# Performance work log

Hardware: AMD Instinct MI355X
Metric: run time of the kernel (lower is better)

Reference implementation:

```python
import jax, jax.numpy as jnp
from jax import lax
import numpy as np

NC = 80      # classes
NM = 32      # mask coefficients
N = 8400     # anchors/boxes
H = 640; W = 640          # output canvas (img_shape)
MH = 160; MW = 160        # prototype mask resolution (img/4)
K = 100                   # max detections after NMS (fixed for jit)
CONF = 0.4
IOU_T = 0.7


def setup_inputs() -> dict:
    key = jax.random.key(0)
    k1, k2, k3, k4, k5, k6 = jax.random.split(key, 6)
    # well-formed boxes x1,y1,x2,y2 in pixel coords
    x1 = jax.random.uniform(k1, (1, 1, N), minval=0.0, maxval=float(W - 120))
    y1 = jax.random.uniform(k2, (1, 1, N), minval=0.0, maxval=float(H - 120))
    wh = jax.random.uniform(k3, (1, 2, N), minval=16.0, maxval=112.0)
    boxes = jnp.concatenate([x1, y1, x1 + wh[:, 0:1], y1 + wh[:, 1:2]], axis=1)
    cls = jax.random.uniform(k4, (1, NC, N), minval=0.0, maxval=0.6)  # some exceed CONF
    coeffs = jax.random.normal(k5, (1, NM, N)) * 0.5
    detect = jnp.concatenate([boxes, cls, coeffs], axis=1)   # [1, 4+NC+NM, N]
    segment = jax.random.normal(k6, (1, NM, MH, MW))
    return {"detect": detect, "segment": segment}


def _per_image(d, proto):
    mi = 4 + NC
    d = d.T                              # [N, 4+NC+NM]
    boxes = d[:, :4]                     # x1,y1,x2,y2
    cls = d[:, 4:mi]
    scores = jnp.max(cls, axis=1)
    cids = jnp.argmax(cls, axis=1)
    coeffs = d[:, mi:]                   # [N, NM]
    valid = scores >= CONF
    # sort by confidence descending (invalid last)
    order = jnp.argsort(jnp.where(valid, -scores, jnp.inf))
    b = boxes[order]; s = scores[order]; v = valid[order]
    c = cids[order]; co = coeffs[order]
    idx = jnp.arange(N)
    area = (b[:, 2] - b[:, 0]) * (b[:, 3] - b[:, 1])
    # greedy class-agnostic NMS (sequential over sorted boxes, vectorized inner)
    def nms_step(keep, i):
        bi = b[i]
        ix1 = jnp.maximum(bi[0], b[:, 0]); iy1 = jnp.maximum(bi[1], b[:, 1])
        ix2 = jnp.minimum(bi[2], b[:, 2]); iy2 = jnp.minimum(bi[3], b[:, 3])
        inter = jnp.maximum(ix2 - ix1, 0.0) * jnp.maximum(iy2 - iy1, 0.0)
        iou = inter / (area[i] + area - inter)
        sup = (iou >= IOU_T) & (idx > i) & keep[i]
        return keep & ~sup, None
    keep, _ = lax.scan(nms_step, v, idx)
    # mask-coefficient matmul for ALL boxes (as in source: masks @ segment_reshaped)
    mlog = co @ proto.reshape(NM, -1)    # [N, MH*MW]
    kept_scores = jnp.where(keep, s, -1.0)
    topv, topi = lax.top_k(kept_scores, K)   # first K survivors (already score-sorted)
    valid_k = topv >= CONF
    bk = b[topi]; ck = c[topi]
    prob = jax.nn.sigmoid(mlog[topi].reshape(K, MH, MW))
    hard = (prob > 0.5).astype(prob.dtype)               # binarize at mask res
    up = jax.image.resize(hard, (K, H, W), method="bilinear")  # upsample to canvas
    maskk = up > 0.0
    ysg = jnp.arange(H)[:, None]; xsg = jnp.arange(W)[None, :]
    onehot = jax.nn.one_hot(ck, NC, dtype=jnp.float32)   # [K, NC]
    bi = bk.astype(jnp.int32)
    # paint objects in descending-score order; each box region is overwritten
    def paint(canvas, inp):
        box, m, oh, vv = inp
        inbox = (xsg >= box[0]) & (xsg < box[2]) & (ysg >= box[1]) & (ysg < box[3]) & vv
        canvas = jnp.where(inbox[..., None],
                           jnp.where((m & inbox)[..., None], oh, 0.0),
                           canvas)
        return canvas, None
    canvas0 = jnp.zeros((H, W, NC), dtype=jnp.float32)
    canvas, _ = lax.scan(paint, canvas0, (bi, maskk, onehot, valid_k))
    return canvas


def reference(detect, segment):
    return jax.vmap(_per_image)(detect, segment)   # [B, H, W, NC]
```

## Files before the change

kernel.cpp:

```cpp
#include <hip/hip_runtime.h>

#define NCLS 80
#define NMK  32
#define NB   8400
#define MH_  160
#define MP   25600
#define IH   640
#define IW   640
#define KTOP 100
#define CONFT 0.4f
#define IOUT 0.7f
#define T_PRE 384
#define TW   (T_PRE/64)

__global__ __launch_bounds__(256) void k_prep(const float* __restrict__ det,
    float* __restrict__ key, int* __restrict__ cid, int* __restrict__ rank,
    int* __restrict__ nvp)
{
  int n = blockIdx.x*256 + threadIdx.x;
  bool valid = false;
  if (n < NB){
    float best = det[4*NB + n];
    int bc = 0;
    #pragma unroll 8
    for (int c = 1; c < NCLS; ++c){
      float v = det[(4+c)*NB + n];
      if (v > best){ best = v; bc = c; }
    }
    cid[n] = bc;
    valid = best >= CONFT;
    key[n] = valid ? -best : __builtin_inff();
    rank[n] = 0;
  }
  unsigned long long bal = __ballot(valid);
  if ((threadIdx.x & 63) == 0)
    nvp[blockIdx.x*4 + (threadIdx.x >> 6)] = (int)__popcll(bal);
}

__global__ __launch_bounds__(256) void k_rank(const float* __restrict__ key, int* __restrict__ rank)
{
  __shared__ float tk[256];
  int n = blockIdx.x*256 + threadIdx.x;
  float kn = (n < NB) ? key[n] : 0.f;
  int j0 = blockIdx.y * 263;
  int j1 = min(j0 + 263, NB);
  int part = 0;
  for (int t0 = j0; t0 < j1; t0 += 256){
    int j = t0 + threadIdx.x;
    tk[threadIdx.x] = (j < NB) ? key[j] : 0.f;
    __syncthreads();
    int lim = min(256, j1 - t0);
    for (int jj = 0; jj < lim; ++jj){
      float kj = tk[jj];
      int jg = t0 + jj;
      part += ((kj < kn) || (kj == kn && jg < n)) ? 1 : 0;
    }
    __syncthreads();
  }
  if (n < NB && part) atomicAdd(&rank[n], part);
}

__global__ __launch_bounds__(256) void k_scatter(const float* __restrict__ det,
    const int* __restrict__ cid, const int* __restrict__ rank,
    int* __restrict__ perm, int* __restrict__ scid, float4* __restrict__ sbox)
{
  int n = blockIdx.x*256 + threadIdx.x;
  if (n >= NB) return;
  int r = rank[n];
  perm[r] = n;
  scid[r] = cid[n];
  float4 b;
  b.x = det[0*NB + n]; b.y = det[1*NB + n];
  b.z = det[2*NB + n]; b.w = det[3*NB + n];
  sbox[r] = b;
}

__global__ __launch_bounds__(64) void k_supmat(const float4* __restrict__ sbox,
    unsigned long long* __restrict__ supmat)
{
  const int lane = threadIdx.x;
  const int ti = blockIdx.x;
  const int tj = blockIdx.y;
  float4 bj = sbox[tj*64 + lane];
  float aj = (bj.z - bj.x) * (bj.w - bj.y);
  float4 bi_all = sbox[ti*64 + lane];
  float ai_all  = (bi_all.z - bi_all.x) * (bi_all.w - bi_all.y);
  const int jg = tj*64 + lane;
  unsigned long long myrow = 0ull;
  #pragma unroll 4
  for (int ii = 0; ii < 64; ++ii){
    float bix = __shfl(bi_all.x, ii, 64);
    float biy = __shfl(bi_all.y, ii, 64);
    float biz = __shfl(bi_all.z, ii, 64);
    float biw = __shfl(bi_all.w, ii, 64);
    float ai  = __shfl(ai_all,  ii, 64);
    float ix1 = fmaxf(bix, bj.x), iy1 = fmaxf(biy, bj.y);
    float ix2 = fminf(biz, bj.z), iy2 = fminf(biw, bj.w);
    float inter = fmaxf(ix2 - ix1, 0.f) * fmaxf(iy2 - iy1, 0.f);
    bool sup = (jg > ti*64 + ii) && (inter / (ai + aj - inter) >= IOUT);
    unsigned long long bal = __ballot(sup);
    if (lane == ii) myrow = bal;
  }
  supmat[(size_t)(ti*64 + lane)*TW + tj] = myrow;
}

__global__ __launch_bounds__(1024) void k_greedy(const float4* __restrict__ sbox,
    const int* __restrict__ scid, const int* __restrict__ perm,
    const unsigned long long* __restrict__ supmat, const int* __restrict__ nvp,
    int* __restrict__ selorig, int4* __restrict__ selbox, int* __restrict__ selcid,
    int* __restrict__ nsel)
{
  __shared__ __align__(16) unsigned long long lsup[T_PRE*TW];
  __shared__ int keptpos[KTOP];
  __shared__ int partial[192];
  __shared__ int s_nv;
  __shared__ int s_found;
  const int tid = threadIdx.x;
  {
    const float4* g4 = (const float4*)supmat;
    float4* l4 = (float4*)lsup;
    for (int idx = tid; idx < (T_PRE*TW)/2; idx += 1024) l4[idx] = g4[idx];
    partial[tid & 191] = 0;
  }
  __syncthreads();
  if (tid < 132) partial[tid] = nvp[tid];
  __syncthreads();
  if (tid < 64){
    int s = partial[tid] + partial[tid + 64] + ((tid + 128 < 192) ? partial[tid + 128] : 0);
    #pragma unroll
    for (int sh = 32; sh > 0; sh >>= 1) s += __shfl_xor(s, sh, 64);
    if (tid == 0) s_nv = s;
  }
  __syncthreads();

  if (tid < 64){
    const int lane = tid;
    const int nv = s_nv;
    unsigned long long keepw = 0ull;
    if (lane < TW){
      int nbits = nv - lane*64;
      if (nbits >= 64) keepw = ~0ull;
      else if (nbits > 0) keepw = (1ull << nbits) - 1ull;
    }
    int found = 0;
    const int lim = min(nv, T_PRE);
    unsigned long long r0 = (lane < TW) ? lsup[0*TW + lane] : 0ull;
    unsigned long long r1 = (lane < TW) ? lsup[1*TW + lane] : 0ull;
    for (int cand = 0; cand < lim; ++cand){
      unsigned long long r2 = (lane < TW && cand + 2 < T_PRE) ? lsup[(cand+2)*TW + lane] : 0ull;
      bool mine = (lane == (cand >> 6)) && ((keepw >> (cand & 63)) & 1ull);
      if (__ballot(mine)){
        if (lane == 0) keptpos[found] = cand;
        found++;
        if (found >= KTOP) break;
        keepw &= ~r0;
      }
      r0 = r1; r1 = r2;
    }
    if (found < KTOP && nv > T_PRE){
      float4 kbA = make_float4(0.f,0.f,0.f,0.f);
      float4 kbB = make_float4(0.f,0.f,0.f,0.f);
      if (lane < found)      kbA = sbox[keptpos[lane]];
      if (lane + 64 < found) kbB = sbox[keptpos[lane + 64]];
      for (int j = T_PRE; j < nv && found < KTOP; ++j){
        float4 bj = sbox[j];
        float ajj = (bj.z - bj.x) * (bj.w - bj.y);
        bool s = false;
        if (lane < found){
          float ka = (kbA.z - kbA.x) * (kbA.w - kbA.y);
          float ix1 = fmaxf(kbA.x, bj.x), iy1 = fmaxf(kbA.y, bj.y);
          float ix2 = fminf(kbA.z, bj.z), iy2 = fminf(kbA.w, bj.w);
          float inter = fmaxf(ix2 - ix1, 0.f) * fmaxf(iy2 - iy1, 0.f);
          s = inter / (ka + ajj - inter) >= IOUT;
        }
        if (lane + 64 < found){
          float ka = (kbB.z - kbB.x) * (kbB.w - kbB.y);
          float ix1 = fmaxf(kbB.x, bj.x), iy1 = fmaxf(kbB.y, bj.y);
          float ix2 = fminf(kbB.z, bj.z), iy2 = fminf(kbB.w, bj.w);
          float inter = fmaxf(ix2 - ix1, 0.f) * fmaxf(iy2 - iy1, 0.f);
          s = s || (inter / (ka + ajj - inter) >= IOUT);
        }
        if (!__ballot(s)){
          if (lane == 0) keptpos[found] = j;
          if (found < 64){ if (lane == found) kbA = bj; }
          else           { if (lane == found - 64) kbB = bj; }
          found++;
        }
      }
    }
    if (lane == 0) s_found = found;
  }
  __syncthreads();
  const int ns = s_found;
  if (tid < ns){
    int si = keptpos[tid];
    float4 b = sbox[si];
    selorig[tid] = perm[si];
    selbox[tid]  = make_int4((int)b.x, (int)b.y, (int)b.z, (int)b.w);
    selcid[tid]  = scid[si];
  }
  if (tid == 0) *nsel = ns;
}

__global__ __launch_bounds__(256) void k_mask(const float* __restrict__ det, const float* __restrict__ proto,
    const int* __restrict__ selorig, const int* __restrict__ nsel, unsigned int* __restrict__ hb)
{
  const int p    = blockIdx.x*256 + threadIdx.x;
  const int lane = threadIdx.x & 63;
  const int wword = (blockIdx.x*256 + (threadIdx.x & ~63)) >> 5;
  float pr[NMK];
  #pragma unroll
  for (int m = 0; m < NMK; ++m) pr[m] = proto[m*MP + p];
  const int ns = *nsel;
  const int k0 = blockIdx.y * 10;
  for (int kk = 0; kk < 10; ++kk){
    int k = k0 + kk;
    if (k >= ns) break;
    int so = selorig[k];
    const float* cf = det + 84*NB + so;
    float acc = 0.f;
    #pragma unroll
    for (int m = 0; m < NMK; ++m) acc = fmaf(cf[(size_t)m*NB], pr[m], acc);
    unsigned long long bal = __ballot(acc > 0.f);
    if (lane == 0)  hb[k*800 + wword]     = (unsigned int)bal;
    if (lane == 32) hb[k*800 + wword + 1] = (unsigned int)(bal >> 32);
  }
}

__global__ __launch_bounds__(256) void k_paint(const int4* __restrict__ selbox, const int* __restrict__ selcid,
    const int* __restrict__ nsel, const unsigned int* __restrict__ hb, float* __restrict__ out)
{
  __shared__ int4  sbx[KTOP];
  __shared__ int   scd[KTOP];
  __shared__ short wcls[IW];
  __shared__ short clist[KTOP];
  __shared__ int   ccount;
  const int y = blockIdx.x;
  const int tid = threadIdx.x;
  const int ns = *nsel;
  if (tid < ns){ sbx[tid] = selbox[tid]; scd[tid] = selcid[tid]; }
  if (tid == 0) ccount = 0;
  __syncthreads();
  if (tid == 0){
    int m = 0;
    for (int k = 0; k < ns; ++k)
      if (y >= sbx[k].y && y < sbx[k].w) clist[m++] = (short)k;
    ccount = m;
  }
  __syncthreads();
  const int m = ccount;
  const int fyi = (y - 2) >> 2;
  const int ylo = max(fyi, 0), yhi = min(fyi + 1, MH_ - 1);
  for (int x = tid; x < IW; x += 256){
    int cls = -1;
    for (int ci = m - 1; ci >= 0; --ci){
      int k = clist[ci];
      int4 b = sbx[k];
      if (x >= b.x && x < b.z){
        int fx = (x - 2) >> 2;
        int xlo = max(fx, 0), xhi = min(fx + 1, MH_ - 1);
        bool on = false;
        for (int ry = ylo; ry <= yhi; ++ry)
          for (int rx = xlo; rx <= xhi; ++rx){
            int pp = ry*MH_ + rx;
            on = on || ((hb[k*800 + (pp >> 5)] >> (pp & 31)) & 1u);
          }
        cls = on ? scd[k] : -1;
        break;
      }
    }
    wcls[x] = (short)cls;
  }
  __syncthreads();
  float4* o4 = (float4*)(out + (size_t)y * (IW*NCLS));
  for (int it = 0; it < 50; ++it){
    int f4 = it*256 + tid;
    int x  = f4 / 20;
    int c  = (f4 % 20) * 4;
    int wc = wcls[x];
    float4 v;
    v.x = (wc == c    ) ? 1.f : 0.f;
    v.y = (wc == c + 1) ? 1.f : 0.f;
    v.z = (wc == c + 2) ? 1.f : 0.f;
    v.w = (wc == c + 3) ? 1.f : 0.f;
    o4[f4] = v;
  }
}

extern "C" void kernel_launch(void* const* d_in, const int* in_sizes, int n_in,
                              void* d_out, int out_size, void* d_ws, size_t ws_size,
                              hipStream_t stream)
{
  const float* det   = (const float*)d_in[0];
  const float* proto = (const float*)d_in[1];
  float* out = (float*)d_out;
  char* w = (char*)d_ws;
  float*  key     = (float*)(w + 0);
  int*    cid     = (int*)  (w + 33600);
  int*    rank    = (int*)  (w + 67200);
  int*    perm    = (int*)  (w + 100800);
  int*    scid    = (int*)  (w + 134400);
  float4* sbox    = (float4*)(w + 168000);
  int*    selorig = (int*)  (w + 302400);
  int4*   selbox  = (int4*) (w + 302800);
  int*    selcid  = (int*)  (w + 304400);
  int*    nsel    = (int*)  (w + 304800);
  int*    nvp     = (int*)  (w + 304832);
  unsigned int* hb = (unsigned int*)(w + 305408);
  unsigned long long* supmat = (unsigned long long*)(w + 625408);

  hipLaunchKernelGGL(k_prep,    dim3(33),      dim3(256),  0, stream, det, key, cid, rank, nvp);
  hipLaunchKernelGGL(k_rank,    dim3(33, 32),  dim3(256),  0, stream, key, rank);
  hipLaunchKernelGGL(k_scatter, dim3(33),      dim3(256),  0, stream, det, cid, rank, perm, scid, sbox);
  hipLaunchKernelGGL(k_supmat,  dim3(TW, TW),  dim3(64),   0, stream, sbox, supmat);
  hipLaunchKernelGGL(k_greedy,  dim3(1),       dim3(1024), 0, stream, sbox, scid, perm, supmat, nvp,
                     selorig, selbox, selcid, nsel);
  hipLaunchKernelGGL(k_mask,    dim3(100, 10), dim3(256),  0, stream, det, proto, selorig, nsel, hb);
  hipLaunchKernelGGL(k_paint,   dim3(640),     dim3(256),  0, stream, selbox, selcid, nsel, hb, out);
}
```

Measured before the change: 220.7 us.

## Fuse seven pipeline kernels into one cooperative persistent kernel with grid syncs

Merges the prep, rank, scatter, suppression-matrix, greedy NMS, mask and paint kernels into a single cooperative kernel of 512 persistent blocks, using grid-wide syncs between stages. This removes six kernel-launch boundaries and their gaps. The rank work is regrouped into larger tiles and the paint stage now builds its per-row candidate list with a wave ballot instead of a serial single-thread loop. In exchange, each stage is limited to the fixed block count, grid syncs add their own cost, and the single-block greedy stage leaves the rest of the GPU idle while the others wait at a barrier.

```diff
diff --git a/kernel.cpp b/kernel.cpp
--- a/kernel.cpp
+++ b/kernel.cpp
@@ -1,4 +1,7 @@
 #include <hip/hip_runtime.h>
+#include <hip/hip_cooperative_groups.h>
+
+namespace cg = cooperative_groups;
 
 #define NCLS 80
 #define NMK  32
@@ -12,278 +15,286 @@
 #define IOUT 0.7f
 #define T_PRE 384
 #define TW   (T_PRE/64)
-
-__global__ __launch_bounds__(256) void k_prep(const float* __restrict__ det,
-    float* __restrict__ key, int* __restrict__ cid, int* __restrict__ rank,
-    int* __restrict__ nvp)
+#define NBLK 512
+
+__global__ __launch_bounds__(256, 2) void k_fused(
+    const float* __restrict__ det, const float* __restrict__ proto,
+    float* __restrict__ key, int* __restrict__ cid, int* __restrict__ rankv,
+    int* __restrict__ perm, int* __restrict__ scid, float4* __restrict__ sbox,
+    unsigned long long* __restrict__ supmat, int* __restrict__ nvp,
+    int* __restrict__ selorig, int4* __restrict__ selbox, int* __restrict__ selcid,
+    int* __restrict__ nsel, unsigned int* __restrict__ hb, float* __restrict__ out)
 {
-  int n = blockIdx.x*256 + threadIdx.x;
-  bool valid = false;
-  if (n < NB){
-    float best = det[4*NB + n];
-    int bc = 0;
-    #pragma unroll 8
-    for (int c = 1; c < NCLS; ++c){
-      float v = det[(4+c)*NB + n];
-      if (v > best){ best = v; bc = c; }
-    }
-    cid[n] = bc;
-    valid = best >= CONFT;
-    key[n] = valid ? -best : __builtin_inff();
-    rank[n] = 0;
-  }
-  unsigned long long bal = __ballot(valid);
-  if ((threadIdx.x & 63) == 0)
-    nvp[blockIdx.x*4 + (threadIdx.x >> 6)] = (int)__popcll(bal);
-}
-
-__global__ __launch_bounds__(256) void k_rank(const float* __restrict__ key, int* __restrict__ rank)
-{
-  __shared__ float tk[256];
-  int n = blockIdx.x*256 + threadIdx.x;
-  float kn = (n < NB) ? key[n] : 0.f;
-  int j0 = blockIdx.y * 263;
-  int j1 = min(j0 + 263, NB);
-  int part = 0;
-  for (int t0 = j0; t0 < j1; t0 += 256){
-    int j = t0 + threadIdx.x;
-    tk[threadIdx.x] = (j < NB) ? key[j] : 0.f;
+  cg::grid_group grid = cg::this_grid();
+  const int bid  = blockIdx.x;
+  const int tid  = threadIdx.x;
+  const int lane = tid & 63;
+  const int wv   = tid >> 6;
+  __shared__ __align__(16) char sbuf[18432];
+  __shared__ int keptpos[KTOP];
+  __shared__ int s_misc[8];
+
+  if (bid < 33){
+    int n = bid*256 + tid;
+    bool valid = false;
+    if (n < NB){
+      float best = det[4*NB + n];
+      int bc = 0;
+      #pragma unroll 8
+      for (int c = 1; c < NCLS; ++c){
+        float v = det[(4+c)*NB + n];
+        if (v > best){ best = v; bc = c; }
+      }
+      cid[n] = bc;
+      valid = best >= CONFT;
+      key[n] = valid ? -best : __builtin_inff();
+      rankv[n] = 0;
+    }
+    unsigned long long bal = __ballot(valid);
+    if (lane == 0) nvp[bid*4 + wv] = (int)__popcll(bal);
+  }
+  grid.sync();
+
+  {
+    float* tk = (float*)sbuf;
+    for (int rt = bid; rt < 528; rt += NBLK){
+      int nb = rt >> 4, js = rt & 15;
+      int n = nb*256 + tid;
+      float kn = (n < NB) ? key[n] : 0.f;
+      int j0 = js*525, j1 = j0 + 525;
+      int part = 0;
+      for (int t0 = j0; t0 < j1; t0 += 256){
+        int j = t0 + tid;
+        tk[tid] = (j < NB) ? key[j] : 0.f;
+        __syncthreads();
+        int lim = min(256, j1 - t0);
+        for (int jj = 0; jj < lim; ++jj){
+          float kj = tk[jj];
+          part += ((kj < kn) || (kj == kn && (t0 + jj) < n)) ? 1 : 0;
+        }
+        __syncthreads();
+      }
+      if (n < NB && part) atomicAdd(&rankv[n], part);
+    }
+  }
+  grid.sync();
+
+  if (bid < 33){
+    int n = bid*256 + tid;
+    if (n < NB){
+      int r = rankv[n];
+      perm[r] = n;
+      scid[r] = cid[n];
+      float4 b;
+      b.x = det[0*NB + n]; b.y = det[1*NB + n];
+      b.z = det[2*NB + n]; b.w = det[3*NB + n];
+      sbox[r] = b;
+    }
+  }
+  grid.sync();
+
+  if (bid < 9){
+    int t = bid*4 + wv;
+    if (t < TW*TW){
+      const int ti = t / TW, tj = t % TW;
+      float4 bj = sbox[tj*64 + lane];
+      float aj = (bj.z - bj.x) * (bj.w - bj.y);
+      float4 bi_all = sbox[ti*64 + lane];
+      float ai_all  = (bi_all.z - bi_all.x) * (bi_all.w - bi_all.y);
+      const int jg = tj*64 + lane;
+      unsigned long long myrow = 0ull;
+      #pragma unroll 4
+      for (int ii = 0; ii < 64; ++ii){
+        float bix = __shfl(bi_all.x, ii, 64);
+        float biy = __shfl(bi_all.y, ii, 64);
+        float biz = __shfl(bi_all.z, ii, 64);
+        float biw = __shfl(bi_all.w, ii, 64);
+        float ai  = __shfl(ai_all,  ii, 64);
+        float ix1 = fmaxf(bix, bj.x), iy1 = fmaxf(biy, bj.y);
+        float ix2 = fminf(biz, bj.z), iy2 = fminf(biw, bj.w);
+        float inter = fmaxf(ix2 - ix1, 0.f) * fmaxf(iy2 - iy1, 0.f);
+        bool sup = (jg > ti*64 + ii) && (inter / (ai + aj - inter) >= IOUT);
+        unsigned long long bal = __ballot(sup);
+        if (lane == ii) myrow = bal;
+      }
+      supmat[(size_t)(ti*64 + lane)*TW + tj] = myrow;
+    }
+  }
+  grid.sync();
+
+  if (bid == 0){
+    unsigned long long* lsup = (unsigned long long*)sbuf;
+    {
+      const float4* g4 = (const float4*)supmat;
+      float4* l4 = (float4*)sbuf;
+      for (int idx = tid; idx < (T_PRE*TW)/2; idx += 256) l4[idx] = g4[idx];
+    }
+    {
+      int v = (tid < 132) ? nvp[tid] : 0;
+      #pragma unroll
+      for (int s = 32; s > 0; s >>= 1) v += __shfl_xor(v, s, 64);
+      if (lane == 0) s_misc[2 + wv] = v;
+    }
     __syncthreads();
-    int lim = min(256, j1 - t0);
-    for (int jj = 0; jj < lim; ++jj){
-      float kj = tk[jj];
-      int jg = t0 + jj;
-      part += ((kj < kn) || (kj == kn && jg < n)) ? 1 : 0;
-    }
+    if (tid == 0) s_misc[0] = s_misc[2] + s_misc[3] + s_misc[4] + s_misc[5];
     __syncthreads();
-  }
-  if (n < NB && part) atomicAdd(&rank[n], part);
-}
-
-__global__ __launch_bounds__(256) void k_scatter(const float* __restrict__ det,
-    const int* __restrict__ cid, const int* __restrict__ rank,
-    int* __restrict__ perm, int* __restrict__ scid, float4* __restrict__ sbox)
-{
-  int n = blockIdx.x*256 + threadIdx.x;
-  if (n >= NB) return;
-  int r = rank[n];
-  perm[r] = n;
-  scid[r] = cid[n];
-  float4 b;
-  b.x = det[0*NB + n]; b.y = det[1*NB + n];
-  b.z = det[2*NB + n]; b.w = det[3*NB + n];
-  sbox[r] = b;
-}
-
-__global__ __launch_bounds__(64) void k_supmat(const float4* __restrict__ sbox,
-    unsigned long long* __restrict__ supmat)
-{
-  const int lane = threadIdx.x;
-  const int ti = blockIdx.x;
-  const int tj = blockIdx.y;
-  float4 bj = sbox[tj*64 + lane];
-  float aj = (bj.z - bj.x) * (bj.w - bj.y);
-  float4 bi_all = sbox[ti*64 + lane];
-  float ai_all  = (bi_all.z - bi_all.x) * (bi_all.w - bi_all.y);
-  const int jg = tj*64 + lane;
-  unsigned long long myrow = 0ull;
-  #pragma unroll 4
-  for (int ii = 0; ii < 64; ++ii){
-    float bix = __shfl(bi_all.x, ii, 64);
-    float biy = __shfl(bi_all.y, ii, 64);
-    float biz = __shfl(bi_all.z, ii, 64);
-    float biw = __shfl(bi_all.w, ii, 64);
-    float ai  = __shfl(ai_all,  ii, 64);
-    float ix1 = fmaxf(bix, bj.x), iy1 = fmaxf(biy, bj.y);
-    float ix2 = fminf(biz, bj.z), iy2 = fminf(biw, bj.w);
-    float inter = fmaxf(ix2 - ix1, 0.f) * fmaxf(iy2 - iy1, 0.f);
-    bool sup = (jg > ti*64 + ii) && (inter / (ai + aj - inter) >= IOUT);
-    unsigned long long bal = __ballot(sup);
-    if (lane == ii) myrow = bal;
-  }
-  supmat[(size_t)(ti*64 + lane)*TW + tj] = myrow;
-}
-
-__global__ __launch_bounds__(1024) void k_greedy(const float4* __restrict__ sbox,
-    const int* __restrict__ scid, const int* __restrict__ perm,
-    const unsigned long long* __restrict__ supmat, const int* __restrict__ nvp,
-    int* __restrict__ selorig, int4* __restrict__ selbox, int* __restrict__ selcid,
-    int* __restrict__ nsel)
-{
-  __shared__ __align__(16) unsigned long long lsup[T_PRE*TW];
-  __shared__ int keptpos[KTOP];
-  __shared__ int partial[192];
-  __shared__ int s_nv;
-  __shared__ int s_found;
-  const int tid = threadIdx.x;
+
+    if (tid < 64){
+      const int nv = s_misc[0];
+      unsigned long long keepw = 0ull;
+      if (lane < TW){
+        int nbits = nv - lane*64;
+        if (nbits >= 64) keepw = ~0ull;
+        else if (nbits > 0) keepw = (1ull << nbits) - 1ull;
+      }
+      int found = 0;
+      const int lim = min(nv, T_PRE);
+      unsigned long long r0 = (lane < TW) ? lsup[0*TW + lane] : 0ull;
+      unsigned long long r1 = (lane < TW) ? lsup[1*TW + lane] : 0ull;
+      for (int cand = 0; cand < lim; ++cand){
+        unsigned long long r2 = (lane < TW && cand + 2 < T_PRE) ? lsup[(cand+2)*TW + lane] : 0ull;
+        bool mine = (lane == (cand >> 6)) && ((keepw >> (cand & 63)) & 1ull);
+        if (__ballot(mine)){
+          if (lane == 0) keptpos[found] = cand;
+          found++;
+          if (found >= KTOP) break;
+          keepw &= ~r0;
+        }
+        r0 = r1; r1 = r2;
+      }
+      if (found < KTOP && nv > T_PRE){
+        float4 kbA = make_float4(0.f,0.f,0.f,0.f);
+        float4 kbB = make_float4(0.f,0.f,0.f,0.f);
+        if (lane < found)      kbA = sbox[keptpos[lane]];
+        if (lane + 64 < found) kbB = sbox[keptpos[lane + 64]];
+        for (int j = T_PRE; j < nv && found < KTOP; ++j){
+          float4 bj = sbox[j];
+          float ajj = (bj.z - bj.x) * (bj.w - bj.y);
+          bool s = false;
+          if (lane < found){
+            float ka = (kbA.z - kbA.x) * (kbA.w - kbA.y);
+            float ix1 = fmaxf(kbA.x, bj.x), iy1 = fmaxf(kbA.y, bj.y);
+            float ix2 = fminf(kbA.z, bj.z), iy2 = fminf(kbA.w, bj.w);
+            float inter = fmaxf(ix2 - ix1, 0.f) * fmaxf(iy2 - iy1, 0.f);
+            s = inter / (ka + ajj - inter) >= IOUT;
+          }
+          if (lane + 64 < found){
+            float ka = (kbB.z - kbB.x) * (kbB.w - kbB.y);
+            float ix1 = fmaxf(kbB.x, bj.x), iy1 = fmaxf(kbB.y, bj.y);
+            float ix2 = fminf(kbB.z, bj.z), iy2 = fminf(kbB.w, bj.w);
+            float inter = fmaxf(ix2 - ix1, 0.f) * fmaxf(iy2 - iy1, 0.f);
+            s = s || (inter / (ka + ajj - inter) >= IOUT);
+          }
+          if (!__ballot(s)){
+            if (lane == 0) keptpos[found] = j;
+            if (found < 64){ if (lane == found) kbA = bj; }
+            else           { if (lane == found - 64) kbB = bj; }
+            found++;
+          }
+        }
+      }
+      if (lane == 0) s_misc[1] = found;
+    }
+    __syncthreads();
+    const int ns = s_misc[1];
+    if (tid < ns){
+      int si = keptpos[tid];
+      float4 b = sbox[si];
+      selorig[tid] = perm[si];
+      selbox[tid]  = make_int4((int)b.x, (int)b.y, (int)b.z, (int)b.w);
+      selcid[tid]  = scid[si];
+    }
+    if (tid == 0) *nsel = ns;
+  }
+  grid.sync();
+
   {
-    const float4* g4 = (const float4*)supmat;
-    float4* l4 = (float4*)lsup;
-    for (int idx = tid; idx < (T_PRE*TW)/2; idx += 1024) l4[idx] = g4[idx];
-    partial[tid & 191] = 0;
-  }
-  __syncthreads();
-  if (tid < 132) partial[tid] = nvp[tid];
-  __syncthreads();
-  if (tid < 64){
-    int s = partial[tid] + partial[tid + 64] + ((tid + 128 < 192) ? partial[tid + 128] : 0);
-    #pragma unroll
-    for (int sh = 32; sh > 0; sh >>= 1) s += __shfl_xor(s, sh, 64);
-    if (tid == 0) s_nv = s;
-  }
-  __syncthreads();
-
-  if (tid < 64){
-    const int lane = tid;
-    const int nv = s_nv;
-    unsigned long long keepw = 0ull;
-    if (lane < TW){
-      int nbits = nv - lane*64;
-      if (nbits >= 64) keepw = ~0ull;
-      else if (nbits > 0) keepw = (1ull << nbits) - 1ull;
-    }
-    int found = 0;
-    const int lim = min(nv, T_PRE);
-    unsigned long long r0 = (lane < TW) ? lsup[0*TW + lane] : 0ull;
-    unsigned long long r1 = (lane < TW) ? lsup[1*TW + lane] : 0ull;
-    for (int cand = 0; cand < lim; ++cand){
-      unsigned long long r2 = (lane < TW && cand + 2 < T_PRE) ? lsup[(cand+2)*TW + lane] : 0ull;
-      bool mine = (lane == (cand >> 6)) && ((keepw >> (cand & 63)) & 1ull);
-      if (__ballot(mine)){
-        if (lane == 0) keptpos[found] = cand;
-        found++;
-        if (found >= KTOP) break;
-        keepw &= ~r0;
-      }
-      r0 = r1; r1 = r2;
-    }
-    if (found < KTOP && nv > T_PRE){
-      float4 kbA = make_float4(0.f,0.f,0.f,0.f);
-      float4 kbB = make_float4(0.f,0.f,0.f,0.f);
-      if (lane < found)      kbA = sbox[keptpos[lane]];
-      if (lane + 64 < found) kbB = sbox[keptpos[lane + 64]];
-      for (int j = T_PRE; j < nv && found < KTOP; ++j){
-        float4 bj = sbox[j];
-        float ajj = (bj.z - bj.x) * (bj.w - bj.y);
-        bool s = false;
-        if (lane < found){
-          float ka = (kbA.z - kbA.x) * (kbA.w - kbA.y);
-          float ix1 = fmaxf(kbA.x, bj.x), iy1 = fmaxf(kbA.y, bj.y);
-          float ix2 = fminf(kbA.z, bj.z), iy2 = fminf(kbA.w, bj.w);
-          float inter = fmaxf(ix2 - ix1, 0.f) * fmaxf(iy2 - iy1, 0.f);
-          s = inter / (ka + ajj - inter) >= IOUT;
+    const int ns = *nsel;
+    for (int t = bid; t < 1000; t += NBLK){
+      int pb = t % 100, ks = t / 100;
+      int p = pb*256 + tid;
+      float pr[NMK];
+      #pragma unroll
+      for (int m = 0; m < NMK; ++m) pr[m] = proto[m*MP + p];
+      int wbase = (pb*256 + (tid & ~63)) >> 5;
+      int k0 = ks*10;
+      for (int kk = 0; kk < 10; ++kk){
+        int k = k0 + kk;
+        if (k >= ns) break;
+        int so = selorig[k];
+        const float* cf = det + 84*NB + so;
+        float acc = 0.f;
+        #pragma unroll
+        for (int m = 0; m < NMK; ++m) acc = fmaf(cf[(size_t)m*NB], pr[m], acc);
+        unsigned long long bal = __ballot(acc > 0.f);
+        if (lane == 0)  hb[k*800 + wbase]     = (unsigned int)bal;
+        if (lane == 32) hb[k*800 + wbase + 1] = (unsigned int)(bal >> 32);
+      }
+    }
+  }
+  grid.sync();
+
+  {
+    int4*  psbx   = (int4*)sbuf;
+    int*   pscd   = (int*)(sbuf + 1600);
+    short* pwcls  = (short*)(sbuf + 2000);
+    short* pclist = (short*)(sbuf + 3280);
+    const int ns = *nsel;
+    for (int t = bid; t < IH; t += NBLK){
+      const int y = t;
+      if (tid < ns){ psbx[tid] = selbox[tid]; pscd[tid] = selcid[tid]; }
+      __syncthreads();
+      if (tid < 64){
+        bool h0 = (tid < ns) && y >= psbx[tid].y && y < psbx[tid].w;
+        unsigned long long m0 = __ballot(h0);
+        if (h0) pclist[(int)__popcll(m0 & ((1ull << tid) - 1ull))] = (short)tid;
+        int k1 = tid + 64;
+        bool h1 = (k1 < ns) && y >= psbx[k1].y && y < psbx[k1].w;
+        unsigned long long m1 = __ballot(h1);
+        int base = (int)__popcll(m0);
+        if (h1) pclist[base + (int)__popcll(m1 & ((1ull << tid) - 1ull))] = (short)k1;
+        if (tid == 0) s_misc[0] = base + (int)__popcll(m1);
+      }
+      __syncthreads();
+      const int m = s_misc[0];
+      const int fyi = (y - 2) >> 2;
+      const int ylo = max(fyi, 0), yhi = min(fyi + 1, MH_ - 1);
+      for (int x = tid; x < IW; x += 256){
+        int cls = -1;
+        for (int ci = m - 1; ci >= 0; --ci){
+          int k = pclist[ci];
+          int4 b = psbx[k];
+          if (x >= b.x && x < b.z){
+            int fx = (x - 2) >> 2;
+            int xlo = max(fx, 0), xhi = min(fx + 1, MH_ - 1);
+            bool on = false;
+            for (int ry = ylo; ry <= yhi; ++ry)
+              for (int rx = xlo; rx <= xhi; ++rx){
+                int pp = ry*MH_ + rx;
+                on = on || ((hb[k*800 + (pp >> 5)] >> (pp & 31)) & 1u);
+              }
+            cls = on ? pscd[k] : -1;
+            break;
+          }
         }
-        if (lane + 64 < found){
-          float ka = (kbB.z - kbB.x) * (kbB.w - kbB.y);
-          float ix1 = fmaxf(kbB.x, bj.x), iy1 = fmaxf(kbB.y, bj.y);
-          float ix2 = fminf(kbB.z, bj.z), iy2 = fminf(kbB.w, bj.w);
-          float inter = fmaxf(ix2 - ix1, 0.f) * fmaxf(iy2 - iy1, 0.f);
-          s = s || (inter / (ka + ajj - inter) >= IOUT);
-        }
-        if (!__ballot(s)){
-          if (lane == 0) keptpos[found] = j;
-          if (found < 64){ if (lane == found) kbA = bj; }
-          else           { if (lane == found - 64) kbB = bj; }
-          found++;
-        }
-      }
-    }
-    if (lane == 0) s_found = found;
-  }
-  __syncthreads();
-  const int ns = s_found;
-  if (tid < ns){
-    int si = keptpos[tid];
-    float4 b = sbox[si];
-    selorig[tid] = perm[si];
-    selbox[tid]  = make_int4((int)b.x, (int)b.y, (int)b.z, (int)b.w);
-    selcid[tid]  = scid[si];
-  }
-  if (tid == 0) *nsel = ns;
-}
-
-__global__ __launch_bounds__(256) void k_mask(const float* __restrict__ det, const float* __restrict__ proto,
-    const int* __restrict__ selorig, const int* __restrict__ nsel, unsigned int* __restrict__ hb)
-{
-  const int p    = blockIdx.x*256 + threadIdx.x;
-  const int lane = threadIdx.x & 63;
-  const int wword = (blockIdx.x*256 + (threadIdx.x & ~63)) >> 5;
-  float pr[NMK];
-  #pragma unroll
-  for (int m = 0; m < NMK; ++m) pr[m] = proto[m*MP + p];
-  const int ns = *nsel;
-  const int k0 = blockIdx.y * 10;
-  for (int kk = 0; kk < 10; ++kk){
-    int k = k0 + kk;
-    if (k >= ns) break;
-    int so = selorig[k];
-    const float* cf = det + 84*NB + so;
-    float acc = 0.f;
-    #pragma unroll
-    for (int m = 0; m < NMK; ++m) acc = fmaf(cf[(size_t)m*NB], pr[m], acc);
-    unsigned long long bal = __ballot(acc > 0.f);
-    if (lane == 0)  hb[k*800 + wword]     = (unsigned int)bal;
-    if (lane == 32) hb[k*800 + wword + 1] = (unsigned int)(bal >> 32);
-  }
-}
-
-__global__ __launch_bounds__(256) void k_paint(const int4* __restrict__ selbox, const int* __restrict__ selcid,
-    const int* __restrict__ nsel, const unsigned int* __restrict__ hb, float* __restrict__ out)
-{
-  __shared__ int4  sbx[KTOP];
-  __shared__ int   scd[KTOP];
-  __shared__ short wcls[IW];
-  __shared__ short clist[KTOP];
-  __shared__ int   ccount;
-  const int y = blockIdx.x;
-  const int tid = threadIdx.x;
-  const int ns = *nsel;
-  if (tid < ns){ sbx[tid] = selbox[tid]; scd[tid] = selcid[tid]; }
-  if (tid == 0) ccount = 0;
-  __syncthreads();
-  if (tid == 0){
-    int m = 0;
-    for (int k = 0; k < ns; ++k)
-      if (y >= sbx[k].y && y < sbx[k].w) clist[m++] = (short)k;
-    ccount = m;
-  }
-  __syncthreads();
-  const int m = ccount;
-  const int fyi = (y - 2) >> 2;
-  const int ylo = max(fyi, 0), yhi = min(fyi + 1, MH_ - 1);
-  for (int x = tid; x < IW; x += 256){
-    int cls = -1;
-    for (int ci = m - 1; ci >= 0; --ci){
-      int k = clist[ci];
-      int4 b = sbx[k];
-      if (x >= b.x && x < b.z){
-        int fx = (x - 2) >> 2;
-        int xlo = max(fx, 0), xhi = min(fx + 1, MH_ - 1);
-        bool on = false;
-        for (int ry = ylo; ry <= yhi; ++ry)
-          for (int rx = xlo; rx <= xhi; ++rx){
-            int pp = ry*MH_ + rx;
-            on = on || ((hb[k*800 + (pp >> 5)] >> (pp & 31)) & 1u);
-          }
-        cls = on ? scd[k] : -1;
-        break;
-      }
-    }
-    wcls[x] = (short)cls;
-  }
-  __syncthreads();
-  float4* o4 = (float4*)(out + (size_t)y * (IW*NCLS));
-  for (int it = 0; it < 50; ++it){
-    int f4 = it*256 + tid;
-    int x  = f4 / 20;
-    int c  = (f4 % 20) * 4;
-    int wc = wcls[x];
-    float4 v;
-    v.x = (wc == c    ) ? 1.f : 0.f;
-    v.y = (wc == c + 1) ? 1.f : 0.f;
-    v.z = (wc == c + 2) ? 1.f : 0.f;
-    v.w = (wc == c + 3) ? 1.f : 0.f;
-    o4[f4] = v;
+        pwcls[x] = (short)cls;
+      }
+      __syncthreads();
+      float4* o4 = (float4*)(out + (size_t)y * (IW*NCLS));
+      for (int it = 0; it < 50; ++it){
+        int f4 = it*256 + tid;
+        int x  = f4 / 20;
+        int c  = (f4 % 20) * 4;
+        int wc = pwcls[x];
+        float4 v;
+        v.x = (wc == c    ) ? 1.f : 0.f;
+        v.y = (wc == c + 1) ? 1.f : 0.f;
+        v.z = (wc == c + 2) ? 1.f : 0.f;
+        v.w = (wc == c + 3) ? 1.f : 0.f;
+        o4[f4] = v;
+      }
+      __syncthreads();
+    }
   }
 }
 
@@ -297,7 +308,7 @@
   char* w = (char*)d_ws;
   float*  key     = (float*)(w + 0);
   int*    cid     = (int*)  (w + 33600);
-  int*    rank    = (int*)  (w + 67200);
+  int*    rankv   = (int*)  (w + 67200);
   int*    perm    = (int*)  (w + 100800);
   int*    scid    = (int*)  (w + 134400);
   float4* sbox    = (float4*)(w + 168000);
@@ -309,12 +320,9 @@
   unsigned int* hb = (unsigned int*)(w + 305408);
   unsigned long long* supmat = (unsigned long long*)(w + 625408);
 
-  hipLaunchKernelGGL(k_prep,    dim3(33),      dim3(256),  0, stream, det, key, cid, rank, nvp);
-  hipLaunchKernelGGL(k_rank,    dim3(33, 32),  dim3(256),  0, stream, key, rank);
-  hipLaunchKernelGGL(k_scatter, dim3(33),      dim3(256),  0, stream, det, cid, rank, perm, scid, sbox);
-  hipLaunchKernelGGL(k_supmat,  dim3(TW, TW),  dim3(64),   0, stream, sbox, supmat);
-  hipLaunchKernelGGL(k_greedy,  dim3(1),       dim3(1024), 0, stream, sbox, scid, perm, supmat, nvp,
-                     selorig, selbox, selcid, nsel);
-  hipLaunchKernelGGL(k_mask,    dim3(100, 10), dim3(256),  0, stream, det, proto, selorig, nsel, hb);
-  hipLaunchKernelGGL(k_paint,   dim3(640),     dim3(256),  0, stream, selbox, selcid, nsel, hb, out);
+  void* args[16] = { (void*)&det, (void*)&proto, (void*)&key, (void*)&cid, (void*)&rankv,
+                     (void*)&perm, (void*)&scid, (void*)&sbox, (void*)&supmat, (void*)&nvp,
+                     (void*)&selorig, (void*)&selbox, (void*)&selcid, (void*)&nsel,
+                     (void*)&hb, (void*)&out };
+  hipLaunchCooperativeKernel((const void*)k_fused, dim3(NBLK), dim3(256), args, 0, stream);
 }
```

Measured after the change: 513.1 us. 132% more time.
